# Performance work log

Measured on AMD Instinct MI355X. Metric: run time of the kernel, lower is better.

The kernel has to match this reference:

```python
import jax, jax.numpy as jnp
import numpy as np
from jax import lax

K = 4  # scan directions

def setup_inputs() -> dict:
    key = jax.random.key(0)
    ks = jax.random.split(key, 8)
    B, D, H, W = 8, 192, 64, 64
    N, R = 16, 6
    return {
        "x": jax.random.normal(ks[0], (B, D, H, W), jnp.float32),
        "x_proj_weight": jax.random.normal(ks[1], (K, R + 2 * N, D), jnp.float32) * (D ** -0.5),
        "dt_projs_weight": jax.random.normal(ks[2], (K, D, R), jnp.float32) * (R ** -0.5),
        "dt_projs_bias": jax.random.normal(ks[3], (K, D), jnp.float32) * 0.1,
        "A_logs": jax.random.uniform(ks[4], (K * D, N), jnp.float32, 0.0, 1.0),
        "Ds": jnp.ones((K * D,), jnp.float32),
        "out_norm_weight": jnp.ones((D,), jnp.float32),
        "out_norm_bias": jnp.zeros((D,), jnp.float32),
    }


def _ss2d_core(x, x_proj_weight, dt_projs_weight, dt_projs_bias, A_logs, Ds,
               out_norm_weight, out_norm_bias):
    B, D, H, W = x.shape
    L = H * W
    N = A_logs.shape[1]
    R = dt_projs_weight.shape[2]

    # ---- CrossScan: 4 traversal orders of the 2D grid ----
    x_flat = x.reshape(B, D, L)                                   # row-major
    x_t = jnp.transpose(x, (0, 1, 3, 2)).reshape(B, D, L)         # col-major
    xs = jnp.stack([x_flat, x_t, x_flat[..., ::-1], x_t[..., ::-1]], axis=1)  # (B,K,D,L)

    # ---- input-dependent projections ----
    x_dbl = jnp.einsum('bkdl,kcd->bkcl', xs, x_proj_weight)       # (B,K,R+2N,L)
    dts, Bs, Cs = jnp.split(x_dbl, [R, R + N], axis=2)            # (B,K,R,L),(B,K,N,L),(B,K,N,L)
    dts = jnp.einsum('bkrl,kdr->bkdl', dts, dt_projs_weight)      # (B,K,D,L)

    A = -jnp.exp(A_logs.astype(jnp.float32)).reshape(K, D, N)     # (K,D,N)
    delta = jax.nn.softplus(dts + dt_projs_bias[None, :, :, None])  # (B,K,D,L)
    u = xs

    # ---- selective scan over L (sequential state recurrence) ----
    def step(h, inp):
        d_t, u_t, b_t, c_t = inp                                   # (B,K,D),(B,K,D),(B,K,N),(B,K,N)
        dA = jnp.exp(d_t[..., None] * A)                           # (B,K,D,N)
        h = dA * h + (d_t * u_t)[..., None] * b_t[:, :, None, :]
        y = jnp.einsum('bkdn,bkn->bkd', h, c_t)
        return h, y

    h0 = jnp.zeros((B, K, D, N), jnp.float32)
    inputs = (jnp.moveaxis(delta, -1, 0), jnp.moveaxis(u, -1, 0),
              jnp.moveaxis(Bs, -1, 0), jnp.moveaxis(Cs, -1, 0))
    _, ys = lax.scan(step, h0, inputs)                             # (L,B,K,D)
    ys = jnp.moveaxis(ys, 0, -1)                                   # (B,K,D,L)
    ys = ys + u * Ds.reshape(K, D)[None, :, :, None]               # skip term D*u

    # ---- CrossMerge: undo flips/transposes and sum the 4 directions ----
    ys2 = ys[:, 0:2] + ys[:, 2:4][..., ::-1]                        # (B,2,D,L)
    y = ys2[:, 0] + jnp.transpose(ys2[:, 1].reshape(B, D, W, H), (0, 1, 3, 2)).reshape(B, D, L)

    # ---- out_norm: LayerNorm over channel dim, NHWC layout ----
    y = jnp.transpose(y.reshape(B, D, H, W), (0, 2, 3, 1))          # (B,H,W,D)
    mean = jnp.mean(y, axis=-1, keepdims=True)
    var = jnp.var(y, axis=-1, keepdims=True)
    y = (y - mean) * lax.rsqrt(var + 1e-5) * out_norm_weight + out_norm_bias
    return y.astype(x.dtype)


def reference(x, x_proj_weight, dt_projs_weight, dt_projs_bias, A_logs, Ds,
              out_norm_weight, out_norm_bias):
    return _ss2d_core(x, x_proj_weight, dt_projs_weight, dt_projs_bias,
                      A_logs, Ds, out_norm_weight, out_norm_bias)
```

## Files before the change

kernel.cpp:

```cpp
#include <hip/hip_runtime.h>
#include <hip/hip_bf16.h>

#define B_  8
#define D_  192
#define H_  64
#define W_  64
#define L_  4096
#define K_  4
#define N_  16
#define R_  6
#define C_  38
#define CP  40
#define CL_ 64
#define NC_ 64

using bf16 = __hip_bfloat16;
typedef float v2f __attribute__((ext_vector_type(2)));
typedef short v8s __attribute__((ext_vector_type(8)));
typedef float f32x4 __attribute__((ext_vector_type(4)));

static __device__ __forceinline__ float softplus_f(float x) {
    return fmaxf(x, 0.f) + __logf(1.f + __expf(-fabsf(x)));
}
static __device__ __forceinline__ float bflo(unsigned u) {
    return __uint_as_float(u << 16);
}

__global__ __launch_bounds__(256) void k_transpose(const float* __restrict__ x,
                                                   bf16* __restrict__ xp0b,
                                                   bf16* __restrict__ xp1b) {
    __shared__ float tile[32][33];
    int bi = blockIdx.x;
    int pg = bi & 127;
    int dg = (bi >> 7) % 6;
    int b  = bi / (128 * 6);
    int tx = threadIdx.x & 31;
    int ty = threadIdx.x >> 5;
    size_t xbase = (size_t)b * D_ * L_;
    #pragma unroll
    for (int i = 0; i < 4; i++) {
        int d = dg * 32 + ty + i * 8;
        tile[ty + i * 8][tx] = x[xbase + (size_t)d * L_ + pg * 32 + tx];
    }
    __syncthreads();
    #pragma unroll
    for (int i = 0; i < 4; i++) {
        int p = pg * 32 + ty + i * 8;
        float v = tile[tx][ty + i * 8];
        bf16 vb = __float2bfloat16(v);
        int d = dg * 32 + tx;
        xp0b[((size_t)b * L_ + p) * D_ + d] = vb;
        int hh = p >> 6, ww = p & 63;
        int r = ww * 64 + hh;
        xp1b[((size_t)b * L_ + r) * D_ + d] = vb;
    }
}

__global__ __launch_bounds__(256) void k_proj(const bf16* __restrict__ xp0b,
                                              const bf16* __restrict__ xp1b,
                                              const float* __restrict__ Wp,
                                              float* __restrict__ xdbl) {
    __shared__ __align__(16) unsigned short xt[64 * 200];
    __shared__ __align__(16) unsigned short wt[48 * 200];
    int blk  = blockIdx.x;
    int tile = blk & 63;
    int bk   = blk >> 6;
    int k    = bk & 3;
    int b    = bk >> 2;
    const bf16* xpb = (k & 1) ? xp1b : xp0b;
    int g0 = (k < 2) ? tile * 64 : (L_ - 64 - tile * 64);

    unsigned* wtu = (unsigned*)wt;
    for (int i = threadIdx.x; i < 1000; i += 256) wtu[3800 + i] = 0u;
    const float2* wsrc = (const float2*)(Wp + (size_t)k * C_ * D_);
    for (int i = threadIdx.x; i < 3648; i += 256) {
        float2 wv2 = wsrc[i];
        int c = i / 96, dp = i % 96;
        bf16 b0 = __float2bfloat16(wv2.x), b1 = __float2bfloat16(wv2.y);
        unsigned pack = ((unsigned)(*(unsigned short*)&b1) << 16) |
                        (unsigned)(*(unsigned short*)&b0);
        wtu[c * 100 + dp] = pack;
    }
    const uint4* src = (const uint4*)(xpb + ((size_t)b * L_ + g0) * D_);
    for (int i = threadIdx.x; i < 1536; i += 256) {
        uint4 v = src[i];
        int row = i / 24, cg = i % 24;
        int rr = (k < 2) ? row : 63 - row;
        *((uint4*)(xt + rr * 200 + cg * 8)) = v;
    }
    __syncthreads();

    int wv   = threadIdx.x >> 6;
    int lane = threadIdx.x & 63;
    int m0   = wv * 16;
    int mrow = lane & 15;
    int kq   = lane >> 4;

    f32x4 acc[3];
    #pragma unroll
    for (int nt = 0; nt < 3; nt++) acc[nt] = (f32x4){0.f, 0.f, 0.f, 0.f};

    const unsigned short* arow = xt + (m0 + mrow) * 200 + kq * 8;
    const unsigned short* brow = wt + mrow * 200 + kq * 8;
    #pragma unroll
    for (int kt = 0; kt < 6; kt++) {
        v8s af = *(const v8s*)(arow + kt * 32);
        #pragma unroll
        for (int nt = 0; nt < 3; nt++) {
            v8s bf = *(const v8s*)(brow + nt * 16 * 200 + kt * 32);
            acc[nt] = __builtin_amdgcn_mfma_f32_16x16x32_bf16(af, bf, acc[nt], 0, 0, 0);
        }
    }

    int l0g = tile * 64;
    #pragma unroll
    for (int nt = 0; nt < 3; nt++) {
        int c = nt * 16 + mrow;
        if (c < C_) {
            #pragma unroll
            for (int r = 0; r < 4; r++) {
                int m = m0 + kq * 4 + r;
                xdbl[((size_t)bk * L_ + l0g + m) * CP + c] = acc[nt][r];
            }
        }
    }
}

__global__ __launch_bounds__(192) void k_pass1(const float* __restrict__ xdbl,
                                               const bf16* __restrict__ xp0b,
                                               const bf16* __restrict__ xp1b,
                                               const float* __restrict__ dtw,
                                               const float* __restrict__ dtb,
                                               const float* __restrict__ Alog,
                                               bf16* __restrict__ Pst,
                                               bf16* __restrict__ Hloc) {
    __shared__ __align__(16) unsigned short ut[CL_ * D_];
    int blk = blockIdx.x;
    int c   = blk & (NC_ - 1);
    int bk  = blk >> 6;
    int k   = bk & 3;
    int b   = bk >> 2;
    int d   = threadIdx.x;

    int l0 = c * CL_;
    const bf16* xpb = (k & 1) ? xp1b : xp0b;
    int base_lu = (k < 2) ? l0 : (L_ - CL_ - l0);
    {
        const uint4* usrc = (const uint4*)(xpb + ((size_t)b * L_ + base_lu) * D_);
        uint4* udst = (uint4*)ut;
        #pragma unroll
        for (int i = 0; i < 8; i++) udst[threadIdx.x + i * 192] = usrc[threadIdx.x + i * 192];
    }

    v2f A2[8];
    #pragma unroll
    for (int i = 0; i < 8; i++) {
        A2[i].x = -__expf(Alog[((size_t)(k * D_ + d)) * N_ + 2*i])   * 1.44269504f;
        A2[i].y = -__expf(Alog[((size_t)(k * D_ + d)) * N_ + 2*i+1]) * 1.44269504f;
    }
    float wr[R_];
    #pragma unroll
    for (int r = 0; r < R_; r++) wr[r] = dtw[(k * D_ + d) * R_ + r];
    float bias = dtb[k * D_ + d];

    v2f h[8];
    #pragma unroll
    for (int i = 0; i < 8; i++) { h[i].x = 0.f; h[i].y = 0.f; }
    float S = 0.f;
    const float* rb = xdbl + ((size_t)bk * L_ + l0) * CP;

    int uidx  = ((k < 2) ? 0 : (CL_ - 1)) * D_ + d;
    int ustep = (k < 2) ? D_ : -D_;
    __syncthreads();

    #pragma unroll 2
    for (int s = 0; s < CL_; s++) {
        const float4* r4 = (const float4*)(rb + s * CP);
        float4 q0 = r4[0], q1 = r4[1], q2 = r4[2], q3 = r4[3], q4 = r4[4], q5 = r4[5];
        float dpre = bias + wr[0]*q0.x + wr[1]*q0.y + wr[2]*q0.z + wr[3]*q0.w
                          + wr[4]*q1.x + wr[5]*q1.y;
        float delta = softplus_f(dpre);
        float u = bflo(ut[uidx]);  uidx += ustep;
        float du = delta * u;
        S += delta;
        v2f Bv[8] = {{q1.z,q1.w},{q2.x,q2.y},{q2.z,q2.w},{q3.x,q3.y},
                     {q3.z,q3.w},{q4.x,q4.y},{q4.z,q4.w},{q5.x,q5.y}};
        #pragma unroll
        for (int i = 0; i < 8; i++) {
            v2f t = A2[i] * delta;
            v2f dA;
            dA.x = __builtin_amdgcn_exp2f(t.x);
            dA.y = __builtin_amdgcn_exp2f(t.y);
            h[i] = dA * h[i] + Bv[i] * du;
        }
    }
    size_t o = ((size_t)blk * D_ + d) * N_;
    #pragma unroll
    for (int i = 0; i < 8; i++) {
        v2f t = A2[i] * S;
        Pst[o + 2*i]   = __float2bfloat16(__builtin_amdgcn_exp2f(t.x));
        Pst[o + 2*i+1] = __float2bfloat16(__builtin_amdgcn_exp2f(t.y));
        Hloc[o + 2*i]   = __float2bfloat16(h[i].x);
        Hloc[o + 2*i+1] = __float2bfloat16(h[i].y);
    }
}

__global__ __launch_bounds__(256) void k_pass2(const bf16* __restrict__ Pst,
                                               const bf16* __restrict__ Hloc,
                                               bf16* __restrict__ Hin) {
    int idx = blockIdx.x * 256 + threadIdx.x;
    int bk  = idx / (D_ * N_);
    int dn  = idx % (D_ * N_);
    float hh = 0.f;
    for (int c = 0; c < NC_; c++) {
        size_t o = ((size_t)bk * NC_ + c) * (D_ * N_) + dn;
        Hin[o] = __float2bfloat16(hh);
        hh = __bfloat162float(Pst[o]) * hh + __bfloat162float(Hloc[o]);
    }
}

__global__ __launch_bounds__(192) void k_pass3(const float* __restrict__ xdbl,
                                               const bf16* __restrict__ xp0b,
                                               const bf16* __restrict__ xp1b,
                                               const float* __restrict__ dtw,
                                               const float* __restrict__ dtb,
                                               const float* __restrict__ Alog,
                                               const float* __restrict__ Dsk,
                                               const bf16* __restrict__ Hin,
                                               bf16* __restrict__ ys) {
    __shared__ __align__(16) unsigned short ut[CL_ * D_];
    int blk = blockIdx.x;
    int c   = blk & (NC_ - 1);
    int bk  = blk >> 6;
    int k   = bk & 3;
    int b   = bk >> 2;
    int d   = threadIdx.x;

    int l0 = c * CL_;
    const bf16* xpb = (k & 1) ? xp1b : xp0b;
    int base_lu = (k < 2) ? l0 : (L_ - CL_ - l0);
    {
        const uint4* usrc = (const uint4*)(xpb + ((size_t)b * L_ + base_lu) * D_);
        uint4* udst = (uint4*)ut;
        #pragma unroll
        for (int i = 0; i < 8; i++) udst[threadIdx.x + i * 192] = usrc[threadIdx.x + i * 192];
    }

    v2f A2[8];
    #pragma unroll
    for (int i = 0; i < 8; i++) {
        A2[i].x = -__expf(Alog[((size_t)(k * D_ + d)) * N_ + 2*i])   * 1.44269504f;
        A2[i].y = -__expf(Alog[((size_t)(k * D_ + d)) * N_ + 2*i+1]) * 1.44269504f;
    }
    float wr[R_];
    #pragma unroll
    for (int r = 0; r < R_; r++) wr[r] = dtw[(k * D_ + d) * R_ + r];
    float bias = dtb[k * D_ + d];
    float DsV  = Dsk[k * D_ + d];

    v2f h[8];
    size_t o = ((size_t)blk * D_ + d) * N_;
    #pragma unroll
    for (int i = 0; i < 8; i++) {
        h[i].x = __bfloat162float(Hin[o + 2*i]);
        h[i].y = __bfloat162float(Hin[o + 2*i+1]);
    }

    const float* rb = xdbl + ((size_t)bk * L_ + l0) * CP;
    bf16* yp = ys + ((size_t)bk * L_ + l0) * D_ + d;
    int uidx  = ((k < 2) ? 0 : (CL_ - 1)) * D_ + d;
    int ustep = (k < 2) ? D_ : -D_;
    __syncthreads();

    #pragma unroll 2
    for (int s = 0; s < CL_; s++) {
        const float4* r4 = (const float4*)(rb + s * CP);
        float4 q0 = r4[0], q1 = r4[1], q2 = r4[2], q3 = r4[3], q4 = r4[4];
        float4 q5 = r4[5], q6 = r4[6], q7 = r4[7], q8 = r4[8], q9 = r4[9];
        float dpre = bias + wr[0]*q0.x + wr[1]*q0.y + wr[2]*q0.z + wr[3]*q0.w
                          + wr[4]*q1.x + wr[5]*q1.y;
        float delta = softplus_f(dpre);
        float u = bflo(ut[uidx]);  uidx += ustep;
        float du = delta * u;
        v2f Bv[8] = {{q1.z,q1.w},{q2.x,q2.y},{q2.z,q2.w},{q3.x,q3.y},
                     {q3.z,q3.w},{q4.x,q4.y},{q4.z,q4.w},{q5.x,q5.y}};
        v2f Cv[8] = {{q5.z,q5.w},{q6.x,q6.y},{q6.z,q6.w},{q7.x,q7.y},
                     {q7.z,q7.w},{q8.x,q8.y},{q8.z,q8.w},{q9.x,q9.y}};
        v2f y2; y2.x = 0.f; y2.y = 0.f;
        #pragma unroll
        for (int i = 0; i < 8; i++) {
            v2f t = A2[i] * delta;
            v2f dA;
            dA.x = __builtin_amdgcn_exp2f(t.x);
            dA.y = __builtin_amdgcn_exp2f(t.y);
            h[i] = dA * h[i] + Bv[i] * du;
            y2   = y2 + h[i] * Cv[i];
        }
        float y = y2.x + y2.y;
        *yp = __float2bfloat16(y + u * DsV);
        yp += D_;
    }
}

__global__ __launch_bounds__(192) void k_merge_ln(const bf16* __restrict__ ys,
                                                  const float* __restrict__ gw,
                                                  const float* __restrict__ gb,
                                                  float* __restrict__ out) {
    int p = blockIdx.x & (L_ - 1);
    int b = blockIdx.x >> 12;
    int d = threadIdx.x;
    int hh = p >> 6, ww = p & 63;
    int l1 = ww * 64 + hh;
    size_t base = (size_t)b * K_ * L_ * D_;
    float v = __bfloat162float(ys[base + ((size_t)0 * L_ + p) * D_ + d])
            + __bfloat162float(ys[base + ((size_t)2 * L_ + (L_ - 1 - p)) * D_ + d])
            + __bfloat162float(ys[base + ((size_t)1 * L_ + l1) * D_ + d])
            + __bfloat162float(ys[base + ((size_t)3 * L_ + (L_ - 1 - l1)) * D_ + d]);
    float s1 = v, s2 = v * v;
    #pragma unroll
    for (int off = 32; off; off >>= 1) {
        s1 += __shfl_down(s1, off);
        s2 += __shfl_down(s2, off);
    }
    __shared__ float aS[3], aQ[3];
    int wid = d >> 6, lane = d & 63;
    if (lane == 0) { aS[wid] = s1; aQ[wid] = s2; }
    __syncthreads();
    float ts1 = aS[0] + aS[1] + aS[2];
    float ts2 = aQ[0] + aQ[1] + aQ[2];
    float mean = ts1 * (1.f / 192.f);
    float var  = ts2 * (1.f / 192.f) - mean * mean;
    float inv  = rsqrtf(var + 1e-5f);
    out[((size_t)b * L_ + p) * D_ + d] = (v - mean) * inv * gw[d] + gb[d];
}

extern "C" void kernel_launch(void* const* d_in, const int* in_sizes, int n_in,
                              void* d_out, int out_size, void* d_ws, size_t ws_size,
                              hipStream_t stream) {
    const float* x    = (const float*)d_in[0];
    const float* Wp   = (const float*)d_in[1];
    const float* dtw  = (const float*)d_in[2];
    const float* dtb  = (const float*)d_in[3];
    const float* Alog = (const float*)d_in[4];
    const float* Dsk  = (const float*)d_in[5];
    const float* gw   = (const float*)d_in[6];
    const float* gb   = (const float*)d_in[7];
    float* out = (float*)d_out;

    char* ws = (char*)d_ws;
    const size_t S1b = (size_t)B_ * L_ * D_ * 2;
    const size_t Sx  = (size_t)B_ * K_ * L_ * CP * 4;
    const size_t Ss  = (size_t)B_ * K_ * NC_ * D_ * N_ * 2;
    char* p = ws;
    bf16*  xp0b = (bf16*)p;   p += S1b;
    bf16*  xp1b = (bf16*)p;   p += S1b;
    float* xdbl = (float*)p;  p += Sx;
    bf16*  Pst  = (bf16*)p;   p += Ss;
    bf16*  Hloc = (bf16*)p;   p += Ss;
    bf16*  Hin  = (bf16*)p;   p += Ss;
    bf16*  ys   = (bf16*)p;

    k_transpose<<<B_ * 6 * 128, 256, 0, stream>>>(x, xp0b, xp1b);
    k_proj<<<B_ * K_ * (L_ / 64), 256, 0, stream>>>(xp0b, xp1b, Wp, xdbl);
    k_pass1<<<B_ * K_ * NC_, 192, 0, stream>>>(xdbl, xp0b, xp1b, dtw, dtb, Alog, Pst, Hloc);
    k_pass2<<<(B_ * K_ * D_ * N_) / 256, 256, 0, stream>>>(Pst, Hloc, Hin);
    k_pass3<<<B_ * K_ * NC_, 192, 0, stream>>>(xdbl, xp0b, xp1b, dtw, dtb, Alog, Dsk, Hin, ys);
    k_merge_ln<<<B_ * L_, 192, 0, stream>>>(ys, gw, gb, out);
}
```

Before: 302.8 us.

## Merge scan passes into one local scan plus decaying inter-chunk correction

The chunked scan used to run the full recurrence twice, once to get chunk-end states and once with carried-in states. Now one scan kernel runs the local recurrence from a zero state, writes partial outputs and chunk summaries, and stores the running delta sum per step. A light correction kernel then adds C·exp(A·S)·h_in to each output and stops early once the carried state has decayed below a threshold across the wavefront. This removes one full pass of the state recurrence. In exchange it writes and reads a large fp32 cumulative-delta buffer, adds a read-modify-write of ys, and approximates by dropping contributions below the decay threshold.

```diff
diff --git a/kernel.cpp b/kernel.cpp
--- a/kernel.cpp
+++ b/kernel.cpp
@@ -126,14 +126,17 @@
     }
 }
 
-__global__ __launch_bounds__(192) void k_pass1(const float* __restrict__ xdbl,
+__global__ __launch_bounds__(192) void k_scanA(const float* __restrict__ xdbl,
                                                const bf16* __restrict__ xp0b,
                                                const bf16* __restrict__ xp1b,
                                                const float* __restrict__ dtw,
                                                const float* __restrict__ dtb,
                                                const float* __restrict__ Alog,
+                                               const float* __restrict__ Dsk,
                                                bf16* __restrict__ Pst,
-                                               bf16* __restrict__ Hloc) {
+                                               bf16* __restrict__ Hloc,
+                                               float* __restrict__ Sbuf,
+                                               bf16* __restrict__ ys) {
     __shared__ __align__(16) unsigned short ut[CL_ * D_];
     int blk = blockIdx.x;
     int c   = blk & (NC_ - 1);
@@ -162,112 +165,16 @@
     #pragma unroll
     for (int r = 0; r < R_; r++) wr[r] = dtw[(k * D_ + d) * R_ + r];
     float bias = dtb[k * D_ + d];
+    float DsV  = Dsk[k * D_ + d];
 
     v2f h[8];
     #pragma unroll
     for (int i = 0; i < 8; i++) { h[i].x = 0.f; h[i].y = 0.f; }
     float S = 0.f;
     const float* rb = xdbl + ((size_t)bk * L_ + l0) * CP;
-
-    int uidx  = ((k < 2) ? 0 : (CL_ - 1)) * D_ + d;
-    int ustep = (k < 2) ? D_ : -D_;
-    __syncthreads();
-
-    #pragma unroll 2
-    for (int s = 0; s < CL_; s++) {
-        const float4* r4 = (const float4*)(rb + s * CP);
-        float4 q0 = r4[0], q1 = r4[1], q2 = r4[2], q3 = r4[3], q4 = r4[4], q5 = r4[5];
-        float dpre = bias + wr[0]*q0.x + wr[1]*q0.y + wr[2]*q0.z + wr[3]*q0.w
-                          + wr[4]*q1.x + wr[5]*q1.y;
-        float delta = softplus_f(dpre);
-        float u = bflo(ut[uidx]);  uidx += ustep;
-        float du = delta * u;
-        S += delta;
-        v2f Bv[8] = {{q1.z,q1.w},{q2.x,q2.y},{q2.z,q2.w},{q3.x,q3.y},
-                     {q3.z,q3.w},{q4.x,q4.y},{q4.z,q4.w},{q5.x,q5.y}};
-        #pragma unroll
-        for (int i = 0; i < 8; i++) {
-            v2f t = A2[i] * delta;
-            v2f dA;
-            dA.x = __builtin_amdgcn_exp2f(t.x);
-            dA.y = __builtin_amdgcn_exp2f(t.y);
-            h[i] = dA * h[i] + Bv[i] * du;
-        }
-    }
-    size_t o = ((size_t)blk * D_ + d) * N_;
-    #pragma unroll
-    for (int i = 0; i < 8; i++) {
-        v2f t = A2[i] * S;
-        Pst[o + 2*i]   = __float2bfloat16(__builtin_amdgcn_exp2f(t.x));
-        Pst[o + 2*i+1] = __float2bfloat16(__builtin_amdgcn_exp2f(t.y));
-        Hloc[o + 2*i]   = __float2bfloat16(h[i].x);
-        Hloc[o + 2*i+1] = __float2bfloat16(h[i].y);
-    }
-}
-
-__global__ __launch_bounds__(256) void k_pass2(const bf16* __restrict__ Pst,
-                                               const bf16* __restrict__ Hloc,
-                                               bf16* __restrict__ Hin) {
-    int idx = blockIdx.x * 256 + threadIdx.x;
-    int bk  = idx / (D_ * N_);
-    int dn  = idx % (D_ * N_);
-    float hh = 0.f;
-    for (int c = 0; c < NC_; c++) {
-        size_t o = ((size_t)bk * NC_ + c) * (D_ * N_) + dn;
-        Hin[o] = __float2bfloat16(hh);
-        hh = __bfloat162float(Pst[o]) * hh + __bfloat162float(Hloc[o]);
-    }
-}
-
-__global__ __launch_bounds__(192) void k_pass3(const float* __restrict__ xdbl,
-                                               const bf16* __restrict__ xp0b,
-                                               const bf16* __restrict__ xp1b,
-                                               const float* __restrict__ dtw,
-                                               const float* __restrict__ dtb,
-                                               const float* __restrict__ Alog,
-                                               const float* __restrict__ Dsk,
-                                               const bf16* __restrict__ Hin,
-                                               bf16* __restrict__ ys) {
-    __shared__ __align__(16) unsigned short ut[CL_ * D_];
-    int blk = blockIdx.x;
-    int c   = blk & (NC_ - 1);
-    int bk  = blk >> 6;
-    int k   = bk & 3;
-    int b   = bk >> 2;
-    int d   = threadIdx.x;
-
-    int l0 = c * CL_;
-    const bf16* xpb = (k & 1) ? xp1b : xp0b;
-    int base_lu = (k < 2) ? l0 : (L_ - CL_ - l0);
-    {
-        const uint4* usrc = (const uint4*)(xpb + ((size_t)b * L_ + base_lu) * D_);
-        uint4* udst = (uint4*)ut;
-        #pragma unroll
-        for (int i = 0; i < 8; i++) udst[threadIdx.x + i * 192] = usrc[threadIdx.x + i * 192];
-    }
-
-    v2f A2[8];
-    #pragma unroll
-    for (int i = 0; i < 8; i++) {
-        A2[i].x = -__expf(Alog[((size_t)(k * D_ + d)) * N_ + 2*i])   * 1.44269504f;
-        A2[i].y = -__expf(Alog[((size_t)(k * D_ + d)) * N_ + 2*i+1]) * 1.44269504f;
-    }
-    float wr[R_];
-    #pragma unroll
-    for (int r = 0; r < R_; r++) wr[r] = dtw[(k * D_ + d) * R_ + r];
-    float bias = dtb[k * D_ + d];
-    float DsV  = Dsk[k * D_ + d];
-
-    v2f h[8];
-    size_t o = ((size_t)blk * D_ + d) * N_;
-    #pragma unroll
-    for (int i = 0; i < 8; i++) {
-        h[i].x = __bfloat162float(Hin[o + 2*i]);
-        h[i].y = __bfloat162float(Hin[o + 2*i+1]);
-    }
-
-    const float* rb = xdbl + ((size_t)bk * L_ + l0) * CP;
-    bf16* yp = ys + ((size_t)bk * L_ + l0) * D_ + d;
+    float* Sp = Sbuf + ((size_t)bk * L_ + l0) * D_ + d;
+    bf16* yp  = ys   + ((size_t)bk * L_ + l0) * D_ + d;
+
     int uidx  = ((k < 2) ? 0 : (CL_ - 1)) * D_ + d;
     int ustep = (k < 2) ? D_ : -D_;
     __syncthreads();
@@ -282,6 +189,8 @@
         float delta = softplus_f(dpre);
         float u = bflo(ut[uidx]);  uidx += ustep;
         float du = delta * u;
+        S += delta;
+        *Sp = S;  Sp += D_;
         v2f Bv[8] = {{q1.z,q1.w},{q2.x,q2.y},{q2.z,q2.w},{q3.x,q3.y},
                      {q3.z,q3.w},{q4.x,q4.y},{q4.z,q4.w},{q5.x,q5.y}};
         v2f Cv[8] = {{q5.z,q5.w},{q6.x,q6.y},{q6.z,q6.w},{q7.x,q7.y},
@@ -300,6 +209,78 @@
         *yp = __float2bfloat16(y + u * DsV);
         yp += D_;
     }
+    size_t o = ((size_t)blk * D_ + d) * N_;
+    #pragma unroll
+    for (int i = 0; i < 8; i++) {
+        v2f t = A2[i] * S;
+        Pst[o + 2*i]   = __float2bfloat16(__builtin_amdgcn_exp2f(t.x));
+        Pst[o + 2*i+1] = __float2bfloat16(__builtin_amdgcn_exp2f(t.y));
+        Hloc[o + 2*i]   = __float2bfloat16(h[i].x);
+        Hloc[o + 2*i+1] = __float2bfloat16(h[i].y);
+    }
+}
+
+__global__ __launch_bounds__(256) void k_pass2(const bf16* __restrict__ Pst,
+                                               const bf16* __restrict__ Hloc,
+                                               bf16* __restrict__ Hin) {
+    int idx = blockIdx.x * 256 + threadIdx.x;
+    int bk  = idx / (D_ * N_);
+    int dn  = idx % (D_ * N_);
+    float hh = 0.f;
+    for (int c = 0; c < NC_; c++) {
+        size_t o = ((size_t)bk * NC_ + c) * (D_ * N_) + dn;
+        Hin[o] = __float2bfloat16(hh);
+        hh = __bfloat162float(Pst[o]) * hh + __bfloat162float(Hloc[o]);
+    }
+}
+
+__global__ __launch_bounds__(192) void k_corr(const float* __restrict__ xdbl,
+                                              const float* __restrict__ Sbuf,
+                                              const float* __restrict__ Alog,
+                                              const bf16* __restrict__ Hin,
+                                              bf16* __restrict__ ys) {
+    int blk = blockIdx.x;
+    int c   = blk & (NC_ - 1);
+    if (c == 0) return;
+    int bk  = blk >> 6;
+    int k   = bk & 3;
+    int d   = threadIdx.x;
+
+    float A2[N_];
+    float aMax = -1e30f;
+    #pragma unroll
+    for (int n = 0; n < N_; n++) {
+        A2[n] = -__expf(Alog[((size_t)(k * D_ + d)) * N_ + n]) * 1.44269504f;
+        aMax = fmaxf(aMax, A2[n]);
+    }
+    float g[N_];
+    size_t o = ((size_t)blk * D_ + d) * N_;
+    #pragma unroll
+    for (int n = 0; n < N_; n++) g[n] = __bfloat162float(Hin[o + n]);
+
+    int l0 = c * CL_;
+    const float* rb = xdbl + ((size_t)bk * L_ + l0) * CP;
+    const float* Sp = Sbuf + ((size_t)bk * L_ + l0) * D_ + d;
+    bf16* yp = ys + ((size_t)bk * L_ + l0) * D_ + d;
+
+    for (int s = 0; s < CL_; s++) {
+        float S = *Sp;  Sp += D_;
+        bool alive = (aMax * S > -18.f);
+        if (__ballot(alive) == 0ull) break;
+        const float4* r4 = (const float4*)(rb + s * CP + 20);
+        float4 c5 = r4[0], c6 = r4[1], c7 = r4[2], c8 = r4[3], c9 = r4[4];
+        float Cv[N_] = {c5.z,c5.w,c6.x,c6.y,c6.z,c6.w,c7.x,c7.y,
+                        c7.z,c7.w,c8.x,c8.y,c8.z,c8.w,c9.x,c9.y};
+        float acc = 0.f;
+        #pragma unroll
+        for (int n = 0; n < N_; n++) {
+            float e = __builtin_amdgcn_exp2f(A2[n] * S);
+            acc = fmaf(Cv[n], e * g[n], acc);
+        }
+        float y = __bfloat162float(*yp) + acc;
+        *yp = __float2bfloat16(y);
+        yp += D_;
+    }
 }
 
 __global__ __launch_bounds__(192) void k_merge_ln(const bf16* __restrict__ ys,
@@ -351,6 +332,7 @@
     const size_t S1b = (size_t)B_ * L_ * D_ * 2;
     const size_t Sx  = (size_t)B_ * K_ * L_ * CP * 4;
     const size_t Ss  = (size_t)B_ * K_ * NC_ * D_ * N_ * 2;
+    const size_t Ssb = (size_t)B_ * K_ * L_ * D_ * 4;
     char* p = ws;
     bf16*  xp0b = (bf16*)p;   p += S1b;
     bf16*  xp1b = (bf16*)p;   p += S1b;
@@ -358,12 +340,14 @@
     bf16*  Pst  = (bf16*)p;   p += Ss;
     bf16*  Hloc = (bf16*)p;   p += Ss;
     bf16*  Hin  = (bf16*)p;   p += Ss;
+    float* Sbuf = (float*)p;  p += Ssb;
     bf16*  ys   = (bf16*)p;
 
     k_transpose<<<B_ * 6 * 128, 256, 0, stream>>>(x, xp0b, xp1b);
     k_proj<<<B_ * K_ * (L_ / 64), 256, 0, stream>>>(xp0b, xp1b, Wp, xdbl);
-    k_pass1<<<B_ * K_ * NC_, 192, 0, stream>>>(xdbl, xp0b, xp1b, dtw, dtb, Alog, Pst, Hloc);
+    k_scanA<<<B_ * K_ * NC_, 192, 0, stream>>>(xdbl, xp0b, xp1b, dtw, dtb, Alog, Dsk,
+                                               Pst, Hloc, Sbuf, ys);
     k_pass2<<<(B_ * K_ * D_ * N_) / 256, 256, 0, stream>>>(Pst, Hloc, Hin);
-    k_pass3<<<B_ * K_ * NC_, 192, 0, stream>>>(xdbl, xp0b, xp1b, dtw, dtb, Alog, Dsk, Hin, ys);
+    k_corr<<<B_ * K_ * NC_, 192, 0, stream>>>(xdbl, Sbuf, Alog, Hin, ys);
     k_merge_ln<<<B_ * L_, 192, 0, stream>>>(ys, gw, gb, out);
 }
```

Result: faster. 265.2 us (-12.4%).
